# Kernel optimization log

Hardware: AMD Instinct MI355X
Metric: run time of the kernel (lower is better)

The kernel has to match this reference:

```python
import jax, jax.numpy as jnp
import numpy as np

# Model dims (scaled-down ModelArgs, ratios preserved)
B, L, Dm = 2, 1024, 1024
H, KVH = 16, 4
HD = Dm // H          # head_dim = 64
N = 64                # ssm_state_dim
E, TOPK = 4, 2        # num_experts, expert_top_k
FF = 4 * Dm           # expert hidden
ROUTER_MIX = np.array([0.5, 0.2, 0.15, 0.15], dtype=np.float32)  # layer_idx=0 -> ssm-heavy


def _rms(x, w, eps=1e-6):
    return x * jax.lax.rsqrt(jnp.mean(x * x, axis=-1, keepdims=True) + eps) * w


def setup_inputs() -> dict:
    key = jax.random.key(0)
    ks = jax.random.split(key, 32)
    f32 = jnp.float32
    def nrm(k, shape, s=0.02):
        return (s * jax.random.normal(k, shape)).astype(f32)
    inp = {
        'x': jax.random.normal(ks[0], (B, L, Dm), dtype=f32),
        'goal_cond': 0.1 * jax.random.normal(ks[1], (B, L, Dm), dtype=f32),
        'mem_out': jax.random.normal(ks[2], (B, L, Dm), dtype=f32),
        'norm1_w': jnp.ones((Dm,), f32),
        'norm2_w': jnp.ones((Dm,), f32),
        'router_w': nrm(ks[3], (Dm, 4)),
        'xproj_w': nrm(ks[4], (Dm, 2 * N + H)),
        'A': (-1.0 + 0.1 * jax.random.normal(ks[5], (H, N))).astype(f32),
        'Dp': jnp.ones((H,), f32),
        'gate_w': nrm(ks[6], (Dm, Dm)),
        'gate_b': jnp.zeros((Dm,), f32),
        'ssd_o_w': nrm(ks[7], (Dm, Dm)),
        'q_w': nrm(ks[8], (Dm, Dm)),
        'k_w': nrm(ks[9], (Dm, KVH * HD)),
        'v_w': nrm(ks[10], (Dm, KVH * HD)),
        'o_w': nrm(ks[11], (Dm, Dm)),
        'qn_w': jnp.ones((HD,), f32),
        'kn_w': jnp.ones((HD,), f32),
        'dw_w': nrm(ks[12], (Dm, 3), 0.3),
        'dw_b': jnp.zeros((Dm,), f32),
        'pw_w': nrm(ks[13], (Dm, Dm)),
        'pw_b': jnp.zeros((Dm,), f32),
        'moe_gate_w': nrm(ks[14], (Dm, E)),
        'e_w1': nrm(ks[15], (E, Dm, 2 * FF)),
        'e_w2': nrm(ks[16], (E, FF, Dm)),
        'e_lin_w': nrm(ks[17], (E, Dm, Dm)),
        'e_lin_b': jnp.zeros((E, Dm), f32),
    }
    return inp


def reference(x, goal_cond, mem_out, norm1_w, norm2_w, router_w, xproj_w, A, Dp,
              gate_w, gate_b, ssd_o_w, q_w, k_w, v_w, o_w, qn_w, kn_w,
              dw_w, dw_b, pw_w, pw_b, moe_gate_w, e_w1, e_w2, e_lin_w, e_lin_b):
    b, l, d = x.shape
    res = x
    xn = _rms(x, norm1_w) + goal_cond

    # --- router over 4 paths ---
    w = jax.nn.softmax(xn @ router_w, axis=-1) * jnp.asarray(ROUTER_MIX, x.dtype)
    w = w / w.sum(axis=-1, keepdims=True)  # [B,L,4]

    # --- SSD (Mamba-2 style selective scan) ---
    ssm = xn @ xproj_w                              # [B,L,2N+H]
    Bs, Cs, db = ssm[..., :N], ssm[..., N:2 * N], ssm[..., 2 * N:]
    delta = jax.nn.softplus(db[..., None] + Bs[..., None, :])   # [B,L,H,N]

    def step(s, dt):                                 # s,dt: [B,H,N]
        s = jnp.exp(dt * A) * s + dt * dt
        return s, s
    _, states = jax.lax.scan(step, jnp.zeros((b, H, N), x.dtype), jnp.moveaxis(delta, 1, 0))
    states = jnp.moveaxis(states, 0, 1)              # [B,L,H,N]
    y = jnp.einsum('blhn,bln->blh', states, Cs)      # contract state dim with C
    xg = xn.reshape(b, l, H, HD)
    y = (y[..., None] + xg * Dp[:, None]).reshape(b, l, d)
    gate = jax.nn.sigmoid(xn @ gate_w + gate_b)
    out_ssd = (y * gate) @ ssd_o_w

    # --- GQA attention with qk-norm + RoPE ---
    q = (xn @ q_w).reshape(b, l, H, HD).transpose(0, 2, 1, 3)      # [B,H,L,hd]
    k = (xn @ k_w).reshape(b, l, KVH, HD).transpose(0, 2, 1, 3)
    v = (xn @ v_w).reshape(b, l, KVH, HD).transpose(0, 2, 1, 3)
    q, k = _rms(q, qn_w), _rms(k, kn_w)
    inv_freq = 1.0 / (10000.0 ** (jnp.arange(0, HD, 2, dtype=jnp.float32) / HD))
    fr = jnp.arange(l, dtype=jnp.float32)[:, None] * inv_freq[None, :]
    emb = jnp.concatenate([fr, fr], axis=-1)
    cos, sin = jnp.cos(emb).astype(x.dtype), jnp.sin(emb).astype(x.dtype)
    def rot(u):
        u1, u2 = jnp.split(u, 2, axis=-1)
        return jnp.concatenate([-u2, u1], axis=-1)
    q = q * cos + rot(q) * sin
    k = k * cos + rot(k) * sin
    k = jnp.repeat(k, H // KVH, axis=1)
    v = jnp.repeat(v, H // KVH, axis=1)
    sc = jnp.einsum('bhqd,bhkd->bhqk', q, k) / jnp.sqrt(jnp.asarray(HD, x.dtype))
    attn = jnp.einsum('bhqk,bhkd->bhqd', jax.nn.softmax(sc, axis=-1), v)
    out_attn = attn.transpose(0, 2, 1, 3).reshape(b, l, d) @ o_w

    # --- depthwise conv3 -> silu -> pointwise conv1 ---
    xp = jnp.pad(xn, ((0, 0), (1, 1), (0, 0)))
    dw = xp[:, :-2] * dw_w[:, 0] + xp[:, 1:-1] * dw_w[:, 1] + xp[:, 2:] * dw_w[:, 2] + dw_b
    out_conv = jax.nn.silu(dw) @ pw_w + pw_b

    mixed = (w[..., 0:1] * out_ssd + w[..., 1:2] * out_attn +
             w[..., 2:3] * out_conv + w[..., 3:4] * mem_out)
    x2 = res + mixed

    # --- dense top-k MoE (experts applied over full x as in source) ---
    gp = jax.nn.softmax(_rms(x2, norm2_w) @ moe_gate_w, axis=-1)     # [B,L,E]
    topp, topi = jax.lax.top_k(gp, TOPK)
    wfull = (jax.nn.one_hot(topi, E, dtype=x.dtype) * topp[..., None]).sum(axis=-2)  # [B,L,E]
    moe = jnp.zeros_like(x2)
    for e in range(E):
        h = x2 @ e_w1[e]                     # [B,L,2*FF]
        a, g = jnp.split(h, 2, axis=-1)
        h = (jax.nn.silu(a) * g) @ e_w2[e]   # [B,L,D]
        eo = h @ e_lin_w[e] + e_lin_b[e]
        moe = moe + wfull[..., e:e + 1] * eo
    return x2 + moe
```

## Files before the change

### kernel.cpp

```cpp
#include <hip/hip_runtime.h>
#include <hip/hip_bf16.h>
#include <cstdint>

typedef unsigned short u16;
typedef __attribute__((ext_vector_type(4))) float f32x4;
typedef __attribute__((ext_vector_type(8))) short s16x8;

#define DEV __device__ __forceinline__

DEV u16 f2bf(float x) {
  unsigned u = __float_as_uint(x);
  u += 0x7FFFu + ((u >> 16) & 1u);
  return (u16)(u >> 16);
}
DEV float bf2f(u16 b) { return __uint_as_float(((unsigned)b) << 16); }

DEV void gload16(const void* g, void* l) {
  __builtin_amdgcn_global_load_lds(
      (const __attribute__((address_space(1))) void*)g,
      (__attribute__((address_space(3))) void*)l, 16, 0, 0);
}

template<bool MAXOP>
DEV float blockRed256(float v) {
  for (int o = 32; o; o >>= 1) {
    float t = __shfl_xor(v, o);
    v = MAXOP ? fmaxf(v, t) : v + t;
  }
  __shared__ float s[4];
  __syncthreads();
  if ((threadIdx.x & 63) == 0) s[threadIdx.x >> 6] = v;
  __syncthreads();
  return MAXOP ? fmaxf(fmaxf(s[0], s[1]), fmaxf(s[2], s[3]))
               : (s[0] + s[1] + s[2] + s[3]);
}

struct WtB { const float* in[8]; u16* out[8]; };
__global__ __launch_bounds__(256) void wtransb_k(WtB wb, int K, int N, int ilv) {
  const float* __restrict__ in = wb.in[blockIdx.z];
  u16* __restrict__ out = wb.out[blockIdx.z];
  __shared__ float t[64][68];
  const int n0 = blockIdx.x * 64, k0 = blockIdx.y * 64;
  const int tt = threadIdx.x;
  const int kl = tt >> 4, nl = (tt & 15) * 4;
#pragma unroll
  for (int i = 0; i < 4; ++i) {
    int k = kl + i * 16;
    float4 v{0.f, 0.f, 0.f, 0.f};
    if (n0 + nl + 3 < N) {
      v = *(const float4*)(in + (long long)(k0 + k) * N + n0 + nl);
    } else {
      for (int j = 0; j < 4; ++j)
        if (n0 + nl + j < N) ((float*)&v)[j] = in[(long long)(k0 + k) * N + n0 + nl + j];
    }
    t[nl + 0][k] = v.x; t[nl + 1][k] = v.y; t[nl + 2][k] = v.z; t[nl + 3][k] = v.w;
  }
  __syncthreads();
  const int n = tt >> 2, kq = (tt & 3) * 16;
  if (n0 + n < N) {
    s16x8 o0, o1;
#pragma unroll
    for (int j = 0; j < 8; ++j) { o0[j] = (short)f2bf(t[n][kq + j]); o1[j] = (short)f2bf(t[n][kq + 8 + j]); }
    int c = n0 + n;
    int r = ilv ? ((((c & 4095) >> 4) << 5) + ((c >> 12) << 4) + (c & 15)) : c;
    u16* op = out + (long long)r * K + k0 + kq;
    *(s16x8*)op = o0; *(s16x8*)(op + 8) = o1;
  }
}

struct GemmP {
  const u16* A; int lda; long long sAz;
  const u16* B; int ldb; long long sBz;
  void* C; int ldc; long long sCz;
  int M, N, K;
  int gqa;
  int czmode;
  const float *p0, *p1, *p2, *p3;
  float scale; int eidx;
  u16 *aux0, *aux1, *aux2;
  const int* cnt;
  const int* s2t;
  int xcdr;
};

template<int EPI, int TN, int PIPE = 0>
__global__ __launch_bounds__(256) void gemm_k(GemmP p) {
  constexpr int NF = TN / 32;
  constexpr int NB = PIPE ? 3 : 2;
  __shared__ u16 Al[NB][128 * 64];
  __shared__ u16 Bl[NB][TN * 64];
  __shared__ float sminv[128];
  int bx = blockIdx.x, by = blockIdx.y, z = blockIdx.z;
  if (p.xcdr) {
    const int nx = gridDim.x, ny = gridDim.y;
    const int chunk = nx >> 3;
    int flat = (blockIdx.z * ny + blockIdx.y) * nx + blockIdx.x;
    int c = flat & 7, i = flat >> 3;
    by = i % ny;
    int rest = i / ny;
    bx = c * chunk + rest % chunk;
    z = rest / chunk;
  }
  const int t = threadIdx.x;
  const int lane = t & 63, wid = t >> 6;
  const int wm = wid >> 1, wn = wid & 1;
  const int m0 = by * 128, n0 = bx * TN;
  if (p.cnt && m0 >= p.cnt[p.eidx + z]) return;
  const int* s2te = p.s2t ? p.s2t + (p.eidx + z) * 2048 : nullptr;

  const u16* Ab = p.A + (long long)z * p.sAz;
  const u16* Bb = p.B + (p.gqa ? (long long)(((z >> 4) << 2) + ((z & 15) >> 2)) * p.sBz
                               : (long long)z * p.sBz);
  const int sr = lane >> 3;
  const int sg = (lane & 7) ^ sr;
  long long pao[4]; int lao[4];
  long long pbo[NF]; int lbo[NF];
#pragma unroll
  for (int c = 0; c < 4; ++c) {
    int rbase = c * 32 + wid * 8;
    int ra = m0 + rbase + sr; if (ra > p.M - 1) ra = p.M - 1;
    if (s2te) ra = s2te[ra];
    pao[c] = (long long)ra * p.lda + sg * 8;
    lao[c] = rbase * 64;
  }
#pragma unroll
  for (int c = 0; c < NF; ++c) {
    int rbase = c * 32 + wid * 8;
    int rb = n0 + rbase + sr; if (rb > p.N - 1) rb = p.N - 1;
    pbo[c] = (long long)rb * p.ldb + sg * 8;
    lbo[c] = rbase * 64;
  }

  if (EPI == 11) {
    int r = t >> 1, h2 = t & 1;
    u16* rp = p.aux0 + (long long)z * p.sAz + (long long)(m0 + r) * 1024 + h2 * 8;
    float mx = -1e30f;
    for (int it = 0; it < 64; ++it) {
      s16x8 v = *(const s16x8*)(rp + it * 16);
#pragma unroll
      for (int q = 0; q < 8; ++q) mx = fmaxf(mx, bf2f((u16)v[q]));
    }
    mx = fmaxf(mx, __shfl_xor(mx, 1));
    float sum = 0.f;
    for (int it = 0; it < 64; ++it) {
      s16x8 v = *(s16x8*)(rp + it * 16);
      s16x8 o;
#pragma unroll
      for (int q = 0; q < 8; ++q) {
        float e = __expf(bf2f((u16)v[q]) - mx);
        sum += e;
        o[q] = (short)f2bf(e);
      }
      *(s16x8*)(rp + it * 16) = o;
    }
    sum += __shfl_xor(sum, 1);
    if (!h2) sminv[r] = 1.f / sum;
    asm volatile("s_waitcnt vmcnt(0)" ::: "memory");
    __syncthreads();
  }

  f32x4 acc[4][NF];
#pragma unroll
  for (int i = 0; i < 4; ++i)
#pragma unroll
    for (int j = 0; j < NF; ++j) acc[i][j] = f32x4{0.f, 0.f, 0.f, 0.f};

  const int lr = lane & 15, lk = lane >> 4;

  if constexpr (PIPE) {
    const int NT = p.K >> 6;
#pragma unroll
    for (int c = 0; c < 4; ++c) gload16(Ab + pao[c], &Al[0][lao[c]]);
#pragma unroll
    for (int c = 0; c < NF; ++c) gload16(Bb + pbo[c], &Bl[0][lbo[c]]);
    if (NT > 1) {
#pragma unroll
      for (int c = 0; c < 4; ++c) gload16(Ab + pao[c] + 64, &Al[1][lao[c]]);
#pragma unroll
      for (int c = 0; c < NF; ++c) gload16(Bb + pbo[c] + 64, &Bl[1][lbo[c]]);
    }
    asm volatile("s_waitcnt vmcnt(6)" ::: "memory");
    __builtin_amdgcn_s_barrier();
    int cur = 0, stg = 2;
    for (int ts = 0; ts < NT; ++ts) {
      if (ts + 2 < NT) {
        long long ko = (long long)(ts + 2) * 64;
#pragma unroll
        for (int c = 0; c < 4; ++c) gload16(Ab + pao[c] + ko, &Al[stg][lao[c]]);
#pragma unroll
        for (int c = 0; c < NF; ++c) gload16(Bb + pbo[c] + ko, &Bl[stg][lbo[c]]);
        asm volatile("s_waitcnt vmcnt(6)" ::: "memory");
      } else {
        asm volatile("s_waitcnt vmcnt(0)" ::: "memory");
      }
#pragma unroll
      for (int kk = 0; kk < 2; ++kk) {
        s16x8 af[4], bfr[NF];
        int g = kk * 4 + lk;
#pragma unroll
        for (int i = 0; i < 4; ++i) {
          int ra = wm * 64 + i * 16 + lr;
          af[i] = *(const s16x8*)&Al[cur][ra * 64 + ((g ^ (ra & 7)) * 8)];
        }
#pragma unroll
        for (int j = 0; j < NF; ++j) {
          int rb = wn * (TN / 2) + j * 16 + lr;
          bfr[j] = *(const s16x8*)&Bl[cur][rb * 64 + ((g ^ (rb & 7)) * 8)];
        }
        __builtin_amdgcn_s_setprio(1);
#pragma unroll
        for (int i = 0; i < 4; ++i)
#pragma unroll
          for (int j = 0; j < NF; ++j)
            acc[i][j] = __builtin_amdgcn_mfma_f32_16x16x32_bf16(af[i], bfr[j], acc[i][j], 0, 0, 0);
        __builtin_amdgcn_s_setprio(0);
      }
      asm volatile("s_waitcnt lgkmcnt(0)" ::: "memory");
      __builtin_amdgcn_s_barrier();
      cur = (cur + 1 == 3) ? 0 : cur + 1;
      stg = (stg + 1 == 3) ? 0 : stg + 1;
    }
  } else {
#pragma unroll
    for (int c = 0; c < 4; ++c) gload16(Ab + pao[c], &Al[0][lao[c]]);
#pragma unroll
    for (int c = 0; c < NF; ++c) gload16(Bb + pbo[c], &Bl[0][lbo[c]]);
    __syncthreads();
    int cur = 0;
    for (int k0 = 0; k0 < p.K; k0 += 64) {
      int nxt = cur ^ 1;
      if (k0 + 64 < p.K) {
#pragma unroll
        for (int c = 0; c < 4; ++c) gload16(Ab + pao[c] + k0 + 64, &Al[nxt][lao[c]]);
#pragma unroll
        for (int c = 0; c < NF; ++c) gload16(Bb + pbo[c] + k0 + 64, &Bl[nxt][lbo[c]]);
      }
#pragma unroll
      for (int kk = 0; kk < 2; ++kk) {
        s16x8 af[4], bfr[NF];
        int g = kk * 4 + lk;
#pragma unroll
        for (int i = 0; i < 4; ++i) {
          int ra = wm * 64 + i * 16 + lr;
          af[i] = *(const s16x8*)&Al[cur][ra * 64 + ((g ^ (ra & 7)) * 8)];
        }
#pragma unroll
        for (int j = 0; j < NF; ++j) {
          int rb = wn * (TN / 2) + j * 16 + lr;
          bfr[j] = *(const s16x8*)&Bl[cur][rb * 64 + ((g ^ (rb & 7)) * 8)];
        }
#pragma unroll
        for (int i = 0; i < 4; ++i)
#pragma unroll
          for (int j = 0; j < NF; ++j)
            acc[i][j] = __builtin_amdgcn_mfma_f32_16x16x32_bf16(af[i], bfr[j], acc[i][j], 0, 0, 0);
      }
      __syncthreads();
      cur = nxt;
    }
  }

  long long cb;
  if (p.czmode == 1) { int b = z >> 4, h = z & 15; cb = (long long)b * 1048576 + h * 64; }
  else cb = (long long)z * p.sCz;
  const int lq = lane >> 4;

  if (EPI == 8) {
#pragma unroll
    for (int i = 0; i < 4; ++i) {
#pragma unroll
      for (int u = 0; u < NF / 2; ++u) {
        int pcol = (n0 >> 1) + wn * (TN / 4) + u * 16 + lr;
#pragma unroll
        for (int q = 0; q < 4; ++q) {
          int row = m0 + wm * 64 + i * 16 + lq * 4 + q;
          float a = acc[i][2 * u][q], gg = acc[i][2 * u + 1][q];
          ((u16*)p.C)[cb + (long long)row * p.ldc + pcol] =
              f2bf(a / (1.f + __expf(-a)) * gg);
        }
      }
    }
    return;
  }
#pragma unroll
  for (int i = 0; i < 4; ++i) {
#pragma unroll
    for (int j = 0; j < NF; ++j) {
      int col = n0 + wn * (TN / 2) + j * 16 + lr;
      if (col >= p.N) continue;
#pragma unroll
      for (int q = 0; q < 4; ++q) {
        int row = m0 + wm * 64 + i * 16 + lq * 4 + q;
        float v = acc[i][j][q];
        if (EPI == 0) {
          ((u16*)p.C)[cb + (long long)row * p.ldc + col] = f2bf(v);
        } else if (EPI == 1) {
          ((float*)p.C)[cb + (long long)row * p.ldc + col] = v;
        } else if (EPI == 5) {
          ((u16*)p.C)[cb + (long long)row * p.ldc + col] = f2bf(v * p.scale);
        } else if (EPI == 9) {
          float add = (z == 2) ? p.p0[col] : 0.f;
          ((float*)p.C)[cb + (long long)row * p.ldc + col] = v + add;
        } else if (EPI == 11) {
          float sc = sminv[wm * 64 + i * 16 + lq * 4 + q];
          ((u16*)p.C)[cb + (long long)row * p.ldc + col] = f2bf(v * sc);
        } else if (EPI == 10) {
          if (col < 1024) {
            float gg = 1.f / (1.f + __expf(-(v + p.p0[col])));
            float yv = p.p1[row * 16 + (col >> 6)] +
                       p.p2[(long long)row * 1024 + col] * p.p3[col >> 6];
            ((u16*)p.C)[(long long)row * p.ldc + col] = f2bf(gg * yv);
          } else {
            int c2 = col - 1024;
            if (c2 < 1024) {
              p.aux0[(long long)row * 1024 + c2] = f2bf(v);
            } else if (c2 < 1280) {
              p.aux1[(long long)row * 256 + (c2 - 1024)] = f2bf(v);
            } else {
              int cc = c2 - 1280;
              int b = row >> 10, l = row & 1023, kvh = cc >> 6, d = cc & 63;
              p.aux2[(((long long)(b * 4 + kvh) * 64 + d) << 10) + l] = f2bf(v);
            }
          }
        }
      }
    }
  }
}

__global__ void rms1router_k(const float* x, const float* goal, const float* w,
                             const float* rw, float* xn, u16* xnb, float* wout) {
  int m = blockIdx.x, t = threadIdx.x;
  const float* xr = x + (long long)m * 1024;
  float v[4]; float ss = 0.f;
#pragma unroll
  for (int i = 0; i < 4; ++i) { v[i] = xr[t + i * 256]; ss += v[i] * v[i]; }
  ss = blockRed256<false>(ss);
  float r = rsqrtf(ss * (1.f / 1024.f) + 1e-6f);
  float a[4] = {0.f, 0.f, 0.f, 0.f};
#pragma unroll
  for (int i = 0; i < 4; ++i) {
    int c = t + i * 256;
    float o = v[i] * r * w[c] + goal[(long long)m * 1024 + c];
    xn[(long long)m * 1024 + c] = o;
    xnb[(long long)m * 1024 + c] = f2bf(o);
    const float* rr = rw + c * 4;
    a[0] += o * rr[0]; a[1] += o * rr[1]; a[2] += o * rr[2]; a[3] += o * rr[3];
  }
#pragma unroll
  for (int j = 0; j < 4; ++j) a[j] = blockRed256<false>(a[j]);
  if (t == 0) {
    float mx = fmaxf(fmaxf(a[0], a[1]), fmaxf(a[2], a[3]));
    float e[4]; float s = 0.f;
    for (int j = 0; j < 4; ++j) { e[j] = __expf(a[j] - mx); s += e[j]; }
    const float mix[4] = {0.5f, 0.2f, 0.15f, 0.15f};
    float ws = 0.f;
    for (int j = 0; j < 4; ++j) { e[j] = e[j] / s * mix[j]; ws += e[j]; }
    for (int j = 0; j < 4; ++j) wout[m * 4 + j] = e[j] / ws;
  }
}

DEV float softplus_f(float x) { return x > 15.f ? x : log1pf(__expf(x)); }

__global__ void scanA_k(const float* ssm, const float* A, float* aprod, float* sloc) {
  int blk = blockIdx.x, n = threadIdx.x;
  int c = blk & 63, h = (blk >> 6) & 15, b = blk >> 10;
  float Ah = A[h * 64 + n];
  float ap = 1.f, s = 0.f;
  int l0 = c * 16;
  for (int j = 0; j < 16; ++j) {
    long long off = (long long)(b * 1024 + l0 + j) * 144;
    float d = softplus_f(ssm[off + 128 + h] + ssm[off + n]);
    float a = __expf(d * Ah);
    s = a * s + d * d;
    ap *= a;
  }
  long long o = (long long)blk * 64 + n;
  aprod[o] = ap; sloc[o] = s;
}

__global__ void scanB_k(const float* aprod, const float* sloc, float* cin) {
  int bh = blockIdx.x, n = threadIdx.x;
  float carry = 0.f;
  for (int c = 0; c < 64; ++c) {
    long long o = (long long)(bh * 64 + c) * 64 + n;
    cin[o] = carry;
    carry = aprod[o] * carry + sloc[o];
  }
}

__global__ void scanC_k(const float* ssm, const float* A, const float* cin, float* ysm) {
  int blk = blockIdx.x, n = threadIdx.x;
  int c = blk & 63, h = (blk >> 6) & 15, b = blk >> 10;
  float Ah = A[h * 64 + n];
  float s = cin[(long long)blk * 64 + n];
  int l0 = c * 16;
  for (int j = 0; j < 16; ++j) {
    long long off = (long long)(b * 1024 + l0 + j) * 144;
    float d = softplus_f(ssm[off + 128 + h] + ssm[off + n]);
    float a = __expf(d * Ah);
    s = a * s + d * d;
    float yv = s * ssm[off + 64 + n];
    for (int o2 = 32; o2; o2 >>= 1) yv += __shfl_xor(yv, o2);
    if (n == 0) ysm[(long long)(b * 1024 + l0 + j) * 16 + h] = yv;
  }
}

__global__ void rtab_k(float2* rt) {
  int i = blockIdx.x * 256 + threadIdx.x;
  int l = i >> 5, f = i & 31;
  float fr = (float)l * powf(10000.f, -(float)f * (1.f / 32.f));
  rt[i] = float2{cosf(fr), sinf(fr)};
}

__global__ void rope_k(const u16* qpre, const u16* kpre, const float* qnw,
                       const float* knw, const float2* rtab, u16* qro, u16* kro) {
  int rid = blockIdx.x * 4 + (threadIdx.x >> 6);
  int lane = threadIdx.x & 63;
  float v; const float* nw; int l; u16* dst;
  if (rid < 32768) {
    int b = rid >> 14, h = (rid >> 10) & 15; l = rid & 1023;
    v = bf2f(qpre[(long long)(b * 1024 + l) * 1024 + h * 64 + lane]);
    nw = qnw; dst = qro + (long long)rid * 64;
  } else {
    int r2 = rid - 32768;
    int b = r2 >> 12, kvh = (r2 >> 10) & 3; l = r2 & 1023;
    v = bf2f(kpre[(long long)(b * 1024 + l) * 256 + kvh * 64 + lane]);
    nw = knw; dst = kro + (long long)r2 * 64;
  }
  float ss = v * v;
  for (int o = 32; o; o >>= 1) ss += __shfl_xor(ss, o);
  float r = rsqrtf(ss * (1.f / 64.f) + 1e-6f);
  float vn = v * r * nw[lane];
  float pt = __shfl_xor(vn, 32);
  float2 cs = rtab[l * 32 + (lane & 31)];
  float o2 = vn * cs.x + ((lane < 32) ? -pt : pt) * cs.y;
  dst[lane] = f2bf(o2);
}

__global__ void conv_k(const float* xn, const float* dww, const float* dwb, u16* outb) {
  int m = blockIdx.x; int l = m & 1023;
#pragma unroll
  for (int i = 0; i < 4; ++i) {
    int d = threadIdx.x + i * 256;
    float xm = l > 0    ? xn[(long long)(m - 1) * 1024 + d] : 0.f;
    float x0 =            xn[(long long)m * 1024 + d];
    float xp = l < 1023 ? xn[(long long)(m + 1) * 1024 + d] : 0.f;
    float dv = xm * dww[d * 3] + x0 * dww[d * 3 + 1] + xp * dww[d * 3 + 2] + dwb[d];
    outb[(long long)m * 1024 + d] = f2bf(dv / (1.f + __expf(-dv)));
  }
}

__global__ void mixmoegate_k(const float* x, const float* w, const float* o3,
                             const float* mem, const float* n2w, const float* mg,
                             float* x2, u16* x2b, float* wf) {
  int m = blockIdx.x, t = threadIdx.x;
  float w0 = w[m * 4], w1 = w[m * 4 + 1], w2 = w[m * 4 + 2], w3 = w[m * 4 + 3];
  float ss = 0.f, a[4] = {0.f, 0.f, 0.f, 0.f};
#pragma unroll
  for (int j = 0; j < 4; ++j) {
    int c = t + j * 256;
    long long i = (long long)m * 1024 + c;
    float v = x[i] + w0 * o3[i] + w1 * o3[i + 2097152] + w2 * o3[i + 4194304] +
              w3 * mem[i];
    x2[i] = v; x2b[i] = f2bf(v);
    ss += v * v;
    float vw = v * n2w[c];
    const float* g = mg + c * 4;
    a[0] += vw * g[0]; a[1] += vw * g[1]; a[2] += vw * g[2]; a[3] += vw * g[3];
  }
  ss = blockRed256<false>(ss);
#pragma unroll
  for (int j = 0; j < 4; ++j) a[j] = blockRed256<false>(a[j]);
  if (t == 0) {
    float r = rsqrtf(ss * (1.f / 1024.f) + 1e-6f);
    float mx = -1e30f;
    for (int j = 0; j < 4; ++j) { a[j] *= r; mx = fmaxf(mx, a[j]); }
    float e[4]; float s = 0.f;
    for (int j = 0; j < 4; ++j) { e[j] = __expf(a[j] - mx); s += e[j]; }
    for (int j = 0; j < 4; ++j) e[j] /= s;
    int i0 = 0;
    for (int j = 1; j < 4; ++j) if (e[j] > e[i0]) i0 = j;
    int i1 = -1;
    for (int j = 0; j < 4; ++j) { if (j == i0) continue; if (i1 < 0 || e[j] > e[i1]) i1 = j; }
    for (int j = 0; j < 4; ++j) wf[m * 4 + j] = (j == i0 || j == i1) ? e[j] : 0.f;
  }
}

__global__ void escan_k(const float* wf, int* cnt, int* s2t, int* t2s) {
  int e = threadIdx.x >> 6, lane = threadIdx.x & 63;
  int base = 0;
  for (int c = 0; c < 32; ++c) {
    int m = c * 64 + lane;
    bool r = wf[m * 4 + e] != 0.f;
    unsigned long long mask = __ballot(r);
    int pre = __popcll(mask & ((1ull << lane) - 1ull));
    if (r) { s2t[e * 2048 + base + pre] = m; t2s[m * 4 + e] = base + pre; }
    else t2s[m * 4 + e] = -1;
    base += __popcll(mask);
  }
  if (lane == 0) cnt[e] = base;
  for (int s = base + lane; s < 2048; s += 64) s2t[e * 2048 + s] = 0;
}

__global__ void final2_k(const float* x2, const float* wf, const int* t2s,
                         const float* t3, const float* elb, float* out) {
  int m = blockIdx.x, c4 = threadIdx.x * 4;
  long long i = (long long)m * 1024 + c4;
  float4 val = *(const float4*)(x2 + i);
#pragma unroll
  for (int e = 0; e < 4; ++e) {
    int s = t2s[m * 4 + e];
    if (s < 0) continue;
    float w = wf[m * 4 + e];
    float4 v = *(const float4*)(t3 + ((long long)e * 2048 + s) * 1024 + c4);
    float4 b = *(const float4*)(elb + e * 1024 + c4);
    val.x += w * (v.x + b.x); val.y += w * (v.y + b.y);
    val.z += w * (v.z + b.z); val.w += w * (v.w + b.w);
  }
  *(float4*)(out + i) = val;
}

extern "C" void kernel_launch(void* const* d_in, const int* in_sizes, int n_in,
                              void* d_out, int out_size, void* d_ws, size_t ws_size,
                              hipStream_t stream) {
  const float* x    = (const float*)d_in[0];
  const float* goal = (const float*)d_in[1];
  const float* mem  = (const float*)d_in[2];
  const float* n1w  = (const float*)d_in[3];
  const float* n2w  = (const float*)d_in[4];
  const float* rw   = (const float*)d_in[5];
  const float* xpw  = (const float*)d_in[6];
  const float* Amat = (const float*)d_in[7];
  const float* Dp   = (const float*)d_in[8];
  const float* gw   = (const float*)d_in[9];
  const float* gb   = (const float*)d_in[10];
  const float* sow  = (const float*)d_in[11];
  const float* qw   = (const float*)d_in[12];
  const float* kw   = (const float*)d_in[13];
  const float* vw   = (const float*)d_in[14];
  const float* ow   = (const float*)d_in[15];
  const float* qnw  = (const float*)d_in[16];
  const float* knw  = (const float*)d_in[17];
  const float* dww  = (const float*)d_in[18];
  const float* dwb  = (const float*)d_in[19];
  const float* pww  = (const float*)d_in[20];
  const float* pwb  = (const float*)d_in[21];
  const float* mgw  = (const float*)d_in[22];
  const float* ew1  = (const float*)d_in[23];
  const float* ew2  = (const float*)d_in[24];
  const float* elw  = (const float*)d_in[25];
  const float* elb  = (const float*)d_in[26];
  float* out = (float*)d_out;

  char* base = (char*)d_ws; size_t off = 0;
  auto alloc = [&](size_t b) { void* p = base + off; off += (b + 255) & ~(size_t)255; return p; };
  float* xn    = (float*)alloc(2048ull * 1024 * 4);
  u16*   xnb   = (u16*)  alloc(2048ull * 1024 * 2);
  float* wr    = (float*)alloc(2048ull * 4 * 4);
  float* ssm   = (float*)alloc(2048ull * 144 * 4);
  float* aprod = (float*)alloc(2048ull * 64 * 4);
  float* sloc  = (float*)alloc(2048ull * 64 * 4);
  float* cin   = (float*)alloc(2048ull * 64 * 4);
  float* ysm   = (float*)alloc(2048ull * 16 * 4);
  u16*   qpre  = (u16*)  alloc(2048ull * 1024 * 2);
  u16*   kpre  = (u16*)  alloc(2048ull * 256 * 2);
  u16*   vT    = (u16*)  alloc(2048ull * 256 * 2);
  u16*   qro   = (u16*)  alloc(2048ull * 1024 * 2);
  u16*   kro   = (u16*)  alloc(2048ull * 256 * 2);
  u16*   SA3   = (u16*)  alloc(3ull * 2048 * 1024 * 2);
  u16*   ssdin = SA3;
  u16*   acat  = SA3 + 2097152;
  u16*   cva   = SA3 + 4194304;
  float* t3    = (float*)base;
  float* x2    = (float*)alloc(2048ull * 1024 * 4);
  u16*   x2b   = (u16*)  alloc(2048ull * 1024 * 2);
  float* wfull = (float*)alloc(2048ull * 4 * 4);
  int*   ecnt  = (int*)  alloc(4 * 4);
  int*   s2t   = (int*)  alloc(4ull * 2048 * 4);
  int*   t2s   = (int*)  alloc(2048ull * 4 * 4);
  float2* rtab = (float2*)alloc(32768ull * 8);
  u16* xpwt  = (u16*)alloc(256ull  * 1024 * 2);
  u16* gqkvt = (u16*)alloc(2560ull * 1024 * 2);
  u16* w3t   = (u16*)alloc(3ull * 1024 * 1024 * 2);
  char*  U1    = (char*) alloc(25165824ull);
  float* outs3 = (float*)U1;
  u16*   t2_4  = (u16*)  U1;
  char* BIG = (char*)alloc(67108864ull);
  u16* scores = (u16*)BIG;
  u16* act4   = (u16*)BIG;
  char* EW = (char*)alloc(33554432ull);
  u16* ew1t  = (u16*)EW;
  u16* ew2t4 = (u16*)EW;
  u16* ewlt4 = (u16*)EW;

  rtab_k<<<128, 256, 0, stream>>>(rtab);
  { WtB wb{}; wb.in[0] = gw;  wb.out[0] = gqkvt;
    wb.in[1] = qw;  wb.out[1] = gqkvt + 1048576ull;
    wb.in[2] = sow; wb.out[2] = w3t;
    wb.in[3] = ow;  wb.out[3] = w3t + 1048576ull;
    wb.in[4] = pww; wb.out[4] = w3t + 2097152ull;
    wtransb_k<<<dim3(16, 16, 5), 256, 0, stream>>>(wb, 1024, 1024, 0); }
  { WtB wb{}; wb.in[0] = kw; wb.out[0] = gqkvt + 2097152ull;
    wb.in[1] = vw; wb.out[1] = gqkvt + 2359296ull;
    wtransb_k<<<dim3(4, 16, 2), 256, 0, stream>>>(wb, 1024, 256, 0); }
  { WtB wb{}; wb.in[0] = xpw; wb.out[0] = xpwt;
    wtransb_k<<<dim3(3, 16, 1), 256, 0, stream>>>(wb, 1024, 144, 0); }

  rms1router_k<<<2048, 256, 0, stream>>>(x, goal, n1w, rw, xn, xnb, wr);

  { GemmP p{}; p.A = xnb; p.lda = 1024; p.B = xpwt; p.ldb = 1024; p.C = ssm; p.ldc = 144;
    p.M = 2048; p.N = 144; p.K = 1024;
    gemm_k<1, 64><<<dim3(3, 16, 1), 256, 0, stream>>>(p); }

  scanA_k<<<2048, 64, 0, stream>>>(ssm, Amat, aprod, sloc);
  scanB_k<<<32, 64, 0, stream>>>(aprod, sloc, cin);
  scanC_k<<<2048, 64, 0, stream>>>(ssm, Amat, cin, ysm);

  { GemmP p{}; p.A = xnb; p.lda = 1024; p.B = gqkvt; p.ldb = 1024; p.C = ssdin; p.ldc = 1024;
    p.M = 2048; p.N = 2560; p.K = 1024; p.p0 = gb; p.p1 = ysm; p.p2 = xn; p.p3 = Dp;
    p.aux0 = qpre; p.aux1 = kpre; p.aux2 = vT;
    gemm_k<10, 64><<<dim3(40, 16, 1), 256, 0, stream>>>(p); }

  rope_k<<<10240, 256, 0, stream>>>(qpre, kpre, qnw, knw, rtab, qro, kro);

  { GemmP p{}; p.A = qro; p.lda = 64; p.sAz = 65536; p.B = kro; p.ldb = 64; p.sBz = 65536;
    p.gqa = 1; p.C = scores; p.ldc = 1024; p.sCz = 1048576;
    p.M = 1024; p.N = 1024; p.K = 64; p.scale = 0.125f;
    gemm_k<5, 128><<<dim3(8, 8, 32), 256, 0, stream>>>(p); }
  { GemmP p{}; p.A = scores; p.lda = 1024; p.sAz = 1048576; p.B = vT; p.ldb = 1024; p.sBz = 65536;
    p.gqa = 1; p.C = acat; p.ldc = 1024; p.czmode = 1; p.aux0 = scores;
    p.M = 1024; p.N = 64; p.K = 1024;
    gemm_k<11, 64><<<dim3(1, 8, 32), 256, 0, stream>>>(p); }

  conv_k<<<2048, 256, 0, stream>>>(xn, dww, dwb, cva);

  { GemmP p{}; p.A = SA3; p.lda = 1024; p.sAz = 2097152; p.B = w3t; p.ldb = 1024;
    p.sBz = 1048576; p.C = outs3; p.ldc = 1024; p.sCz = 2097152;
    p.M = 2048; p.N = 1024; p.K = 1024; p.p0 = pwb;
    gemm_k<9, 64><<<dim3(16, 16, 3), 256, 0, stream>>>(p); }

  mixmoegate_k<<<2048, 256, 0, stream>>>(x, wr, outs3, mem, n2w, mgw, x2, x2b, wfull);
  escan_k<<<1, 256, 0, stream>>>(wfull, ecnt, s2t, t2s);

  for (int pr = 0; pr < 2; ++pr) {
    int e0 = pr * 2;
    { WtB wb{}; wb.in[0] = ew1 + (long long)e0 * 8388608; wb.out[0] = ew1t;
      wb.in[1] = ew1 + (long long)(e0 + 1) * 8388608; wb.out[1] = ew1t + 8388608ull;
      wtransb_k<<<dim3(128, 16, 2), 256, 0, stream>>>(wb, 1024, 8192, 1); }
    GemmP p{}; p.A = x2b; p.lda = 1024; p.sAz = 0; p.B = ew1t; p.ldb = 1024; p.sBz = 8192ll * 1024;
    p.C = act4 + (long long)e0 * (2048ll * 4096); p.ldc = 4096; p.sCz = 2048ll * 4096;
    p.M = 2048; p.N = 8192; p.K = 1024; p.eidx = e0; p.cnt = ecnt; p.s2t = s2t; p.xcdr = 1;
    gemm_k<8, 64, 1><<<dim3(128, 16, 2), 256, 0, stream>>>(p);
  }
  { WtB wb{};
    for (int e = 0; e < 4; ++e) {
      wb.in[e] = ew2 + (long long)e * 4194304;
      wb.out[e] = ew2t4 + (long long)e * (1024ll * 4096);
    }
    wtransb_k<<<dim3(16, 64, 4), 256, 0, stream>>>(wb, 4096, 1024, 0); }
  { GemmP p{}; p.A = act4; p.lda = 4096; p.sAz = 2048ll * 4096; p.B = ew2t4; p.ldb = 4096;
    p.sBz = 1024ll * 4096; p.C = t2_4; p.ldc = 1024; p.sCz = 2048ll * 1024;
    p.M = 2048; p.N = 1024; p.K = 4096; p.cnt = ecnt; p.xcdr = 1;
    gemm_k<0, 64, 1><<<dim3(16, 16, 4), 256, 0, stream>>>(p); }
  { WtB wb{};
    for (int e = 0; e < 4; ++e) {
      wb.in[e] = elw + (long long)e * 1048576;
      wb.out[e] = ewlt4 + (long long)e * (1024ll * 1024);
    }
    wtransb_k<<<dim3(16, 16, 4), 256, 0, stream>>>(wb, 1024, 1024, 0); }
  { GemmP p{}; p.A = t2_4; p.lda = 1024; p.sAz = 2048ll * 1024; p.B = ewlt4; p.ldb = 1024;
    p.sBz = 1024ll * 1024; p.C = t3; p.ldc = 1024; p.sCz = 2048ll * 1024;
    p.M = 2048; p.N = 1024; p.K = 1024; p.cnt = ecnt; p.xcdr = 1;
    gemm_k<1, 64, 1><<<dim3(16, 16, 4), 256, 0, stream>>>(p); }

  final2_k<<<2048, 256, 0, stream>>>(x2, wfull, t2s, t3, elb, out);
}
```

Baseline: 648.2 us.

## Group MoE GEMM tiles per XCD and shrink pipeline to double buffering

The block-index remap for the MoE GEMMs now groups G consecutive M-tiles within each XCD's N-column chunk, so blocks on the same XCD share A and B tiles in L2. G is set to 4, 2 and 4 for the three expert GEMMs. The pipelined path also goes from a three-stage LDS ring to a two-stage double buffer with an extra barrier per K step, which cuts LDS use and may raise occupancy. The cost is less prefetch depth to hide global-load latency.

```diff
diff --git a/kernel.cpp b/kernel.cpp
--- a/kernel.cpp
+++ b/kernel.cpp
@@ -86,20 +86,21 @@
 template<int EPI, int TN, int PIPE = 0>
 __global__ __launch_bounds__(256) void gemm_k(GemmP p) {
   constexpr int NF = TN / 32;
-  constexpr int NB = PIPE ? 3 : 2;
-  __shared__ u16 Al[NB][128 * 64];
-  __shared__ u16 Bl[NB][TN * 64];
+  __shared__ u16 Al[2][128 * 64];
+  __shared__ u16 Bl[2][TN * 64];
   __shared__ float sminv[128];
   int bx = blockIdx.x, by = blockIdx.y, z = blockIdx.z;
   if (p.xcdr) {
     const int nx = gridDim.x, ny = gridDim.y;
-    const int chunk = nx >> 3;
+    const int chunk = nx >> 3, G = p.xcdr;
     int flat = (blockIdx.z * ny + blockIdx.y) * nx + blockIdx.x;
     int c = flat & 7, i = flat >> 3;
-    by = i % ny;
-    int rest = i / ny;
-    bx = c * chunk + rest % chunk;
-    z = rest / chunk;
+    int byi = i % G; i /= G;
+    int bxi = i % chunk; i /= chunk;
+    int bg = i % (ny / G); i /= (ny / G);
+    by = bg * G + byi;
+    bx = c * chunk + bxi;
+    z = i;
   }
   const int t = threadIdx.x;
   const int lane = t & 63, wid = t >> 6;
@@ -173,26 +174,19 @@
     for (int c = 0; c < 4; ++c) gload16(Ab + pao[c], &Al[0][lao[c]]);
 #pragma unroll
     for (int c = 0; c < NF; ++c) gload16(Bb + pbo[c], &Bl[0][lbo[c]]);
-    if (NT > 1) {
-#pragma unroll
-      for (int c = 0; c < 4; ++c) gload16(Ab + pao[c] + 64, &Al[1][lao[c]]);
-#pragma unroll
-      for (int c = 0; c < NF; ++c) gload16(Bb + pbo[c] + 64, &Bl[1][lbo[c]]);
-    }
-    asm volatile("s_waitcnt vmcnt(6)" ::: "memory");
-    __builtin_amdgcn_s_barrier();
-    int cur = 0, stg = 2;
     for (int ts = 0; ts < NT; ++ts) {
-      if (ts + 2 < NT) {
-        long long ko = (long long)(ts + 2) * 64;
-#pragma unroll
-        for (int c = 0; c < 4; ++c) gload16(Ab + pao[c] + ko, &Al[stg][lao[c]]);
-#pragma unroll
-        for (int c = 0; c < NF; ++c) gload16(Bb + pbo[c] + ko, &Bl[stg][lbo[c]]);
+      const int cur = ts & 1;
+      if (ts + 1 < NT) {
+        long long ko = (long long)(ts + 1) * 64;
+#pragma unroll
+        for (int c = 0; c < 4; ++c) gload16(Ab + pao[c] + ko, &Al[cur ^ 1][lao[c]]);
+#pragma unroll
+        for (int c = 0; c < NF; ++c) gload16(Bb + pbo[c] + ko, &Bl[cur ^ 1][lbo[c]]);
         asm volatile("s_waitcnt vmcnt(6)" ::: "memory");
       } else {
         asm volatile("s_waitcnt vmcnt(0)" ::: "memory");
       }
+      __builtin_amdgcn_s_barrier();
 #pragma unroll
       for (int kk = 0; kk < 2; ++kk) {
         s16x8 af[4], bfr[NF];
@@ -217,8 +211,6 @@
       }
       asm volatile("s_waitcnt lgkmcnt(0)" ::: "memory");
       __builtin_amdgcn_s_barrier();
-      cur = (cur + 1 == 3) ? 0 : cur + 1;
-      stg = (stg + 1 == 3) ? 0 : stg + 1;
     }
   } else {
 #pragma unroll
@@ -650,7 +642,7 @@
       wtransb_k<<<dim3(128, 16, 2), 256, 0, stream>>>(wb, 1024, 8192, 1); }
     GemmP p{}; p.A = x2b; p.lda = 1024; p.sAz = 0; p.B = ew1t; p.ldb = 1024; p.sBz = 8192ll * 1024;
     p.C = act4 + (long long)e0 * (2048ll * 4096); p.ldc = 4096; p.sCz = 2048ll * 4096;
-    p.M = 2048; p.N = 8192; p.K = 1024; p.eidx = e0; p.cnt = ecnt; p.s2t = s2t; p.xcdr = 1;
+    p.M = 2048; p.N = 8192; p.K = 1024; p.eidx = e0; p.cnt = ecnt; p.s2t = s2t; p.xcdr = 4;
     gemm_k<8, 64, 1><<<dim3(128, 16, 2), 256, 0, stream>>>(p);
   }
   { WtB wb{};
@@ -661,7 +653,7 @@
     wtransb_k<<<dim3(16, 64, 4), 256, 0, stream>>>(wb, 4096, 1024, 0); }
   { GemmP p{}; p.A = act4; p.lda = 4096; p.sAz = 2048ll * 4096; p.B = ew2t4; p.ldb = 4096;
     p.sBz = 1024ll * 4096; p.C = t2_4; p.ldc = 1024; p.sCz = 2048ll * 1024;
-    p.M = 2048; p.N = 1024; p.K = 4096; p.cnt = ecnt; p.xcdr = 1;
+    p.M = 2048; p.N = 1024; p.K = 4096; p.cnt = ecnt; p.xcdr = 2;
     gemm_k<0, 64, 1><<<dim3(16, 16, 4), 256, 0, stream>>>(p); }
   { WtB wb{};
     for (int e = 0; e < 4; ++e) {
@@ -671,7 +663,7 @@
     wtransb_k<<<dim3(16, 16, 4), 256, 0, stream>>>(wb, 1024, 1024, 0); }
   { GemmP p{}; p.A = t2_4; p.lda = 1024; p.sAz = 2048ll * 1024; p.B = ewlt4; p.ldb = 1024;
     p.sBz = 1024ll * 1024; p.C = t3; p.ldc = 1024; p.sCz = 2048ll * 1024;
-    p.M = 2048; p.N = 1024; p.K = 1024; p.cnt = ecnt; p.xcdr = 1;
+    p.M = 2048; p.N = 1024; p.K = 1024; p.cnt = ecnt; p.xcdr = 4;
     gemm_k<1, 64, 1><<<dim3(16, 16, 4), 256, 0, stream>>>(p); }
 
   final2_k<<<2048, 256, 0, stream>>>(x2, wfull, t2s, t3, elb, out);
```

After: 567.9 us. 12.4% less time.
